# Performance work log

Hardware: AMD Instinct MI355X
Metric: run time of the kernel (lower is better)

## Reference

```python
import jax, jax.numpy as jnp
import numpy as np

DIM = 2048
HEADS = 16
HD = DIM // HEADS  # 128
EPS = 1e-5


def layernorm(t, w, b):
    # FloatLayerNorm: LayerNorm computed in float32 over last dim
    t32 = t.astype(jnp.float32)
    mu = jnp.mean(t32, axis=-1, keepdims=True)
    var = jnp.mean(jnp.square(t32 - mu), axis=-1, keepdims=True)
    y = (t32 - mu) * jax.lax.rsqrt(var + EPS)
    return (y * w + b).astype(t.dtype)


def rope(t, f_real, f_imag):
    # t: [b, s, h, hd]; frequencies in cis form, sliced to seq length
    b, s, h, hd = t.shape
    tr = t.astype(jnp.float32).reshape(b, s, h, hd // 2, 2)
    xr, xi = tr[..., 0], tr[..., 1]
    fr = f_real[:s][None, :, None, :]  # [1, s, 1, hd/2]
    fi = f_imag[:s][None, :, None, :]
    o_r = xr * fr - xi * fi
    o_i = xr * fi + xi * fr
    return jnp.stack([o_r, o_i], axis=-1).reshape(b, s, h, hd).astype(t.dtype)


def proj_norm_rope(t, Wq, Wk, Wv, qn_w, qn_b, kn_w, kn_b, f_real, f_imag):
    b, s, _ = t.shape
    q = layernorm(t @ Wq, qn_w, qn_b).reshape(b, s, HEADS, HD)
    k = layernorm(t @ Wk, kn_w, kn_b).reshape(b, s, HEADS, HD)
    v = (t @ Wv).reshape(b, s, HEADS, HD)
    q = rope(q, f_real, f_imag)
    k = rope(k, f_real, f_imag)
    return q, k, v


def sdpa(q, k, v, scale):
    # q,k,v: [b, s, h, hd] -> out [b, s, h, hd]
    scores = jnp.einsum('bqhd,bkhd->bhqk', q, k) * scale
    probs = jax.nn.softmax(scores, axis=-1)
    return jnp.einsum('bhqk,bkhd->bqhd', probs, v)


def setup_inputs() -> dict:
    key = jax.random.key(0)
    ks = jax.random.split(key, 14)
    d = {
        'c': jax.random.normal(ks[0], (2, 256, DIM), jnp.float32),
        'x': jax.random.normal(ks[1], (2, 1792, DIM), jnp.float32),
        'f_real': jax.random.normal(ks[2], (2048, HD // 2), jnp.float32),
        'f_imag': jax.random.normal(ks[3], (2048, HD // 2), jnp.float32),
    }
    sc = 1.0 / np.sqrt(DIM)
    for i, name in enumerate(['Wq', 'Wk', 'Wv', 'Wo', 'W2q', 'W2k', 'W2v', 'W2o']):
        d[name] = jax.random.normal(ks[4 + i], (DIM, DIM), jnp.float32) * sc
    for name in ['qn_w', 'kn_w', 'q2n_w', 'k2n_w']:
        d[name] = jnp.ones((DIM,), jnp.float32)
    for name in ['qn_b', 'kn_b', 'q2n_b', 'k2n_b']:
        d[name] = jnp.zeros((DIM,), jnp.float32)
    return d


def reference(c, x, f_real, f_imag, Wq, Wk, Wv, Wo, W2q, W2k, W2v, W2o,
              qn_w, qn_b, kn_w, kn_b, q2n_w, q2n_b, k2n_w, k2n_b):
    s1 = c.shape[1]
    c_q, c_k, c_v = proj_norm_rope(c, Wq, Wk, Wv, qn_w, qn_b, kn_w, kn_b, f_real, f_imag)
    x_q, x_k, x_v = proj_norm_rope(x, W2q, W2k, W2v, q2n_w, q2n_b, k2n_w, k2n_b, f_real, f_imag)
    q = jnp.concatenate([c_q, x_q], axis=1)
    k = jnp.concatenate([c_k, x_k], axis=1)
    v = jnp.concatenate([c_v, x_v], axis=1)
    out = sdpa(q, k, v, scale=1.0 / np.sqrt(HD))  # scale_by_num_heads=True
    b, s, _, _ = out.shape
    out = out.reshape(b, s, DIM)
    c_out = out[:, :s1] @ Wo
    x_out = out[:, s1:] @ W2o
    return c_out, x_out
```

## Files before the change

kernel.cpp:

```cpp
#include <hip/hip_runtime.h>

typedef __attribute__((ext_vector_type(8))) short short8;
typedef __attribute__((ext_vector_type(4))) float f32x4;
typedef __attribute__((ext_vector_type(16))) float f32x16;

#define DEV __device__ __forceinline__

DEV unsigned short f2bf(float f) {
  unsigned int u; __builtin_memcpy(&u, &f, 4);
  u = (u + 0x7FFFu + ((u >> 16) & 1u)) >> 16;
  return (unsigned short)u;
}
DEV float bf2f(unsigned short h) {
  unsigned int u = ((unsigned int)h) << 16;
  float f; __builtin_memcpy(&f, &u, 4);
  return f;
}
DEV unsigned int cvtpk(float lo, float hi_) {
  unsigned int r;
  asm("v_cvt_pk_bf16_f32 %0, %1, %2" : "=v"(r) : "v"(lo), "v"(hi_));
  return r;
}

DEV void gload_lds16(const void* g, void* l) {
  __builtin_amdgcn_global_load_lds(
      (const __attribute__((address_space(1))) void*)g,
      (__attribute__((address_space(3))) void*)l, 16, 0, 0);
}

DEV f32x16 mfma32(short8 a, short8 b, f32x16 c) {
  return __builtin_amdgcn_mfma_f32_32x32x16_bf16(a, b, c, 0, 0, 0);
}
DEV f32x4 mfma16(short8 a, short8 b, f32x4 c) {
  return __builtin_amdgcn_mfma_f32_16x16x32_bf16(a, b, c, 0, 0, 0);
}

__global__ __launch_bounds__(256) void conv_tb(const float* __restrict__ c,
                                               const float* __restrict__ x,
                                               unsigned short* __restrict__ tb) {
  int row = blockIdx.x;
  int b = row >> 11, s = row & 2047;
  const float* src = (s < 256) ? (c + (size_t)(b * 256 + s) * 2048)
                               : (x + (size_t)(b * 1792 + (s - 256)) * 2048);
  int t = threadIdx.x;
  float4 v0 = *(const float4*)&src[t * 8];
  float4 v1 = *(const float4*)&src[t * 8 + 4];
  union { unsigned short us[8]; uint4 u; } pk;
  pk.us[0] = f2bf(v0.x); pk.us[1] = f2bf(v0.y); pk.us[2] = f2bf(v0.z); pk.us[3] = f2bf(v0.w);
  pk.us[4] = f2bf(v1.x); pk.us[5] = f2bf(v1.y); pk.us[6] = f2bf(v1.z); pk.us[7] = f2bf(v1.w);
  *(uint4*)&tb[(size_t)row * 2048 + t * 8] = pk.u;
}

__global__ __launch_bounds__(256) void trans_w(
    const float* __restrict__ w0, const float* __restrict__ w1,
    const float* __restrict__ w2, const float* __restrict__ w3,
    const float* __restrict__ w4, const float* __restrict__ w5,
    const float* __restrict__ w6, const float* __restrict__ w7,
    unsigned short* __restrict__ dstbase) {
  const float* W;
  switch (blockIdx.z) {
    case 0: W = w0; break; case 1: W = w1; break; case 2: W = w2; break; case 3: W = w3; break;
    case 4: W = w4; break; case 5: W = w5; break; case 6: W = w6; break; default: W = w7; break;
  }
  unsigned short* Wt = dstbase + (size_t)blockIdx.z * 2048 * 2048;
  __shared__ float tile[64][65];
  int n0 = blockIdx.x * 64, k0 = blockIdx.y * 64;
  int j = threadIdx.x & 63, i0 = threadIdx.x >> 6;
#pragma unroll
  for (int p = 0; p < 16; ++p) {
    int i = i0 + p * 4;
    tile[i][j] = W[(size_t)(k0 + i) * 2048 + n0 + j];
  }
  __syncthreads();
#pragma unroll
  for (int p = 0; p < 16; ++p) {
    int i = i0 + p * 4;
    Wt[(size_t)(n0 + i) * 2048 + k0 + j] = f2bf(tile[j][i]);
  }
}

DEV void stage_A8(char* ldsAbase, const unsigned short* gtile, int mh, int wid, int lane) {
#pragma unroll
  for (int p = 0; p < 2; ++p) {
    int row0 = mh * 64 + p * 128 + wid * 8;
    int row = row0 + (lane >> 3);
    int u = (lane & 7) ^ (row & 7);
    gload_lds16(gtile + (size_t)row * 2048 + u * 8, ldsAbase + row0 * 128);
  }
}
DEV void stage_B8(char* ldsBbase, const unsigned short* gtile, int nh, int wid, int lane) {
#pragma unroll
  for (int p = 0; p < 2; ++p) {
    int idx = p * 8 + wid;
    int row0 = (idx >> 2) * 64 + nh * 32 + (idx & 3) * 8;
    int row = row0 + (lane >> 3);
    int u = (lane & 7) ^ (row & 7);
    gload_lds16(gtile + (size_t)row * 2048 + u * 8, ldsBbase + row0 * 128);
  }
}

__global__ __launch_bounds__(512, 2) void gemm_qkv3_8ph(
    const unsigned short* __restrict__ A,
    const unsigned short* __restrict__ Wt,
    unsigned short* __restrict__ out) {
  extern __shared__ __align__(16) char ldsc[];
  const size_t M2 = 2048ull * 2048ull;
  int bid = blockIdx.x;
  int sw = (bid & 7) * 48 + (bid >> 3);
  const int which = sw >> 7;
  const int rem = sw & 127;
  const int m0 = (rem >> 3) * 256, n0 = (rem & 7) * 256;
  const unsigned short* Bt = Wt + (size_t)(((m0 & 2047) < 256) ? which : which + 4) * M2;
  unsigned short* C = out + (size_t)which * (4096ull * 2048ull);
  const int tid = threadIdx.x, wid = tid >> 6, lane = tid & 63;
  const int g = lane >> 4, l15 = lane & 15;
  const int wm = wid >> 2, wn = wid & 3;
  const unsigned short* gA = A + (size_t)m0 * 2048;
  const unsigned short* gB = Bt + (size_t)n0 * 2048;

  f32x4 acc[8][4] = {};

  stage_A8(ldsc, gA, 0, wid, lane);
  stage_A8(ldsc, gA, 1, wid, lane);
  stage_B8(ldsc + 32768, gB, 0, wid, lane);
  stage_B8(ldsc + 32768, gB, 1, wid, lane);
  stage_A8(ldsc + 65536, gA + 64, 0, wid, lane);
  stage_B8(ldsc + 98304, gB + 64, 0, wid, lane);
  asm volatile("s_waitcnt vmcnt(4)" ::: "memory");
  __builtin_amdgcn_s_barrier();

  const int NT = 32;
#pragma unroll 1
  for (int t = 0; t < NT; ++t) {
    const int bufOff = (t & 1) << 16;
    char* Ab = ldsc + bufOff;
    char* Bb = ldsc + 32768 + bufOff;
    char* An = ldsc + (bufOff ^ 65536);
    char* Bn = ldsc + 32768 + (bufOff ^ 65536);
    short8 af[4][2], bf0[2][2], bf1[2][2];

#pragma unroll
    for (int m4 = 0; m4 < 4; ++m4)
#pragma unroll
      for (int k2 = 0; k2 < 2; ++k2) {
        int row = wm * 128 + m4 * 16 + l15;
        af[m4][k2] = *(const short8*)(Ab + row * 128 + (((k2 * 4 + g) ^ (row & 7)) << 4));
      }
#pragma unroll
    for (int n2 = 0; n2 < 2; ++n2)
#pragma unroll
      for (int k2 = 0; k2 < 2; ++k2) {
        int row = wn * 64 + n2 * 16 + l15;
        bf0[n2][k2] = *(const short8*)(Bb + row * 128 + (((k2 * 4 + g) ^ (row & 7)) << 4));
      }
    if (t + 1 < NT) stage_B8(Bn, gB + (t + 1) * 64, 1, wid, lane);
    __builtin_amdgcn_s_barrier();
    asm volatile("s_waitcnt lgkmcnt(0)" ::: "memory");
    __builtin_amdgcn_sched_barrier(0);
    __builtin_amdgcn_s_setprio(1);
#pragma unroll
    for (int m4 = 0; m4 < 4; ++m4)
#pragma unroll
      for (int n2 = 0; n2 < 2; ++n2)
#pragma unroll
        for (int k2 = 0; k2 < 2; ++k2)
          acc[m4][n2] = mfma16(af[m4][k2], bf0[n2][k2], acc[m4][n2]);
    __builtin_amdgcn_s_setprio(0);
    __builtin_amdgcn_s_barrier();

#pragma unroll
    for (int n2 = 0; n2 < 2; ++n2)
#pragma unroll
      for (int k2 = 0; k2 < 2; ++k2) {
        int row = wn * 64 + 32 + n2 * 16 + l15;
        bf1[n2][k2] = *(const short8*)(Bb + row * 128 + (((k2 * 4 + g) ^ (row & 7)) << 4));
      }
    if (t + 1 < NT) stage_A8(An, gA + (t + 1) * 64, 1, wid, lane);
    __builtin_amdgcn_s_barrier();
    asm volatile("s_waitcnt lgkmcnt(0)" ::: "memory");
    __builtin_amdgcn_sched_barrier(0);
    __builtin_amdgcn_s_setprio(1);
#pragma unroll
    for (int m4 = 0; m4 < 4; ++m4)
#pragma unroll
      for (int n2 = 0; n2 < 2; ++n2)
#pragma unroll
        for (int k2 = 0; k2 < 2; ++k2)
          acc[m4][2 + n2] = mfma16(af[m4][k2], bf1[n2][k2], acc[m4][2 + n2]);
    __builtin_amdgcn_s_setprio(0);
    __builtin_amdgcn_s_barrier();

#pragma unroll
    for (int m4 = 0; m4 < 4; ++m4)
#pragma unroll
      for (int k2 = 0; k2 < 2; ++k2) {
        int row = wm * 128 + 64 + m4 * 16 + l15;
        af[m4][k2] = *(const short8*)(Ab + row * 128 + (((k2 * 4 + g) ^ (row & 7)) << 4));
      }
    if (t + 2 < NT) stage_A8(Ab, gA + (t + 2) * 64, 0, wid, lane);
    __builtin_amdgcn_s_barrier();
    asm volatile("s_waitcnt lgkmcnt(0)" ::: "memory");
    __builtin_amdgcn_sched_barrier(0);
    __builtin_amdgcn_s_setprio(1);
#pragma unroll
    for (int m4 = 0; m4 < 4; ++m4)
#pragma unroll
      for (int n2 = 0; n2 < 2; ++n2)
#pragma unroll
        for (int k2 = 0; k2 < 2; ++k2)
          acc[4 + m4][n2] = mfma16(af[m4][k2], bf0[n2][k2], acc[4 + m4][n2]);
    __builtin_amdgcn_s_setprio(0);
    __builtin_amdgcn_s_barrier();

    if (t + 2 < NT) stage_B8(Bb, gB + (t + 2) * 64, 0, wid, lane);
    __builtin_amdgcn_s_barrier();
    __builtin_amdgcn_s_setprio(1);
#pragma unroll
    for (int m4 = 0; m4 < 4; ++m4)
#pragma unroll
      for (int n2 = 0; n2 < 2; ++n2)
#pragma unroll
        for (int k2 = 0; k2 < 2; ++k2)
          acc[4 + m4][2 + n2] = mfma16(af[m4][k2], bf1[n2][k2], acc[4 + m4][2 + n2]);
    __builtin_amdgcn_s_setprio(0);
    if (t + 2 < NT) {
      asm volatile("s_waitcnt vmcnt(4)" ::: "memory");
    } else if (t + 1 < NT) {
      asm volatile("s_waitcnt vmcnt(0)" ::: "memory");
    }
    __builtin_amdgcn_s_barrier();
  }

#pragma unroll
  for (int mh = 0; mh < 2; ++mh)
#pragma unroll
    for (int m4 = 0; m4 < 4; ++m4)
#pragma unroll
      for (int r = 0; r < 4; ++r) {
        int row = m0 + wm * 128 + mh * 64 + m4 * 16 + 4 * g + r;
#pragma unroll
        for (int nh = 0; nh < 2; ++nh)
#pragma unroll
          for (int n2 = 0; n2 < 2; ++n2)
            C[(size_t)row * 2048 + n0 + wn * 64 + nh * 32 + n2 * 16 + l15] =
                f2bf(acc[mh * 4 + m4][nh * 2 + n2][r]);
      }
}

__global__ __launch_bounds__(256) void gemm_out(
    const unsigned short* __restrict__ A,
    const unsigned short* __restrict__ B1t,
    const unsigned short* __restrict__ B2t,
    float* __restrict__ Co) {
  __shared__ __align__(16) unsigned short As[128 * 32];
  __shared__ __align__(16) unsigned short Bs[128 * 32];
  const int m0 = blockIdx.y * 128, n0 = blockIdx.x * 128;
  const unsigned short* Bt = ((m0 & 2047) < 256) ? B1t : B2t;
  const int tid = threadIdx.x, wid = tid >> 6, lane = tid & 63;
  const int g = lane >> 4, l15 = lane & 15;
  const int wm = wid >> 1, wn = wid & 1;
  const int srow = lane >> 2, skk = (lane & 3) * 8;
  f32x4 acc[4][4] = {};
  for (int k0 = 0; k0 < 2048; k0 += 32) {
#pragma unroll
    for (int rep = 0; rep < 2; ++rep) {
      int ia = wid * 2 + rep;
      gload_lds16(&A[(size_t)(m0 + ia * 16 + srow) * 2048 + k0 + skk], (char*)As + ia * 1024);
      gload_lds16(&Bt[(size_t)(n0 + ia * 16 + srow) * 2048 + k0 + skk], (char*)Bs + ia * 1024);
    }
    __syncthreads();
    short8 a[4], bb[4];
#pragma unroll
    for (int mf = 0; mf < 4; ++mf) a[mf] = *(const short8*)&As[(wm * 64 + mf * 16 + l15) * 32 + g * 8];
#pragma unroll
    for (int nf = 0; nf < 4; ++nf) bb[nf] = *(const short8*)&Bs[(wn * 64 + nf * 16 + l15) * 32 + g * 8];
#pragma unroll
    for (int mf = 0; mf < 4; ++mf)
#pragma unroll
      for (int nf = 0; nf < 4; ++nf)
        acc[mf][nf] = __builtin_amdgcn_mfma_f32_16x16x32_bf16(a[mf], bb[nf], acc[mf][nf], 0, 0, 0);
    __syncthreads();
  }
#pragma unroll
  for (int mf = 0; mf < 4; ++mf)
#pragma unroll
    for (int r = 0; r < 4; ++r) {
      int row = m0 + wm * 64 + mf * 16 + 4 * g + r;
      int b = row >> 11, s = row & 2047;
      size_t dst = (s < 256) ? ((size_t)b * 256 + s) * 2048
                             : 1048576ull + ((size_t)b * 1792 + (s - 256)) * 2048;
#pragma unroll
      for (int nf = 0; nf < 4; ++nf)
        Co[dst + n0 + wn * 64 + nf * 16 + l15] = acc[mf][nf][r];
    }
}

__global__ __launch_bounds__(256) void ln_rope(
    const unsigned short* __restrict__ P,
    const float* __restrict__ w1, const float* __restrict__ b1,
    const float* __restrict__ w2, const float* __restrict__ b2,
    const float* __restrict__ fre, const float* __restrict__ fim,
    unsigned short* __restrict__ Oa, float oscale) {
  int row = blockIdx.x;
  int b = row >> 11, s = row & 2047;
  int pos = (s < 256) ? s : s - 256;
  const float* w = (s < 256) ? w1 : w2;
  const float* bb = (s < 256) ? b1 : b2;
  int t = threadIdx.x, lane = t & 63, wid = t >> 6;
  int col = t * 8;
  uint4 raw = *(const uint4*)&P[(size_t)row * 2048 + col];
  const unsigned short* rp = (const unsigned short*)&raw;
  float xv[8];
#pragma unroll
  for (int j = 0; j < 8; ++j) xv[j] = bf2f(rp[j]);
  float s1 = 0.f, s2 = 0.f;
#pragma unroll
  for (int j = 0; j < 8; ++j) { s1 += xv[j]; s2 += xv[j] * xv[j]; }
#pragma unroll
  for (int off = 32; off; off >>= 1) { s1 += __shfl_xor(s1, off); s2 += __shfl_xor(s2, off); }
  __shared__ float red1[4], red2[4];
  if (lane == 0) { red1[wid] = s1; red2[wid] = s2; }
  __syncthreads();
  s1 = red1[0] + red1[1] + red1[2] + red1[3];
  s2 = red2[0] + red2[1] + red2[2] + red2[3];
  float mean = s1 * (1.f / 2048.f);
  float var = s2 * (1.f / 2048.f) - mean * mean;
  float rs = rsqrtf(var + 1e-5f);
  float4 wv0 = *(const float4*)&w[col], wv1 = *(const float4*)&w[col + 4];
  float4 bv0 = *(const float4*)&bb[col], bv1 = *(const float4*)&bb[col + 4];
  float y[8];
  y[0] = (xv[0] - mean) * rs * wv0.x + bv0.x; y[1] = (xv[1] - mean) * rs * wv0.y + bv0.y;
  y[2] = (xv[2] - mean) * rs * wv0.z + bv0.z; y[3] = (xv[3] - mean) * rs * wv0.w + bv0.w;
  y[4] = (xv[4] - mean) * rs * wv1.x + bv1.x; y[5] = (xv[5] - mean) * rs * wv1.y + bv1.y;
  y[6] = (xv[6] - mean) * rs * wv1.z + bv1.z; y[7] = (xv[7] - mean) * rs * wv1.w + bv1.w;
#pragma unroll
  for (int j = 0; j < 8; ++j) y[j] *= oscale;
  int hd0 = col & 127;
  int i0 = hd0 >> 1;
  float4 fr = *(const float4*)&fre[(size_t)pos * 64 + i0];
  float4 fi = *(const float4*)&fim[(size_t)pos * 64 + i0];
  union { unsigned short us[8]; uint4 u; } pk;
  pk.us[0] = f2bf(y[0] * fr.x - y[1] * fi.x); pk.us[1] = f2bf(y[0] * fi.x + y[1] * fr.x);
  pk.us[2] = f2bf(y[2] * fr.y - y[3] * fi.y); pk.us[3] = f2bf(y[2] * fi.y + y[3] * fr.y);
  pk.us[4] = f2bf(y[4] * fr.z - y[5] * fi.z); pk.us[5] = f2bf(y[4] * fi.z + y[5] * fr.z);
  pk.us[6] = f2bf(y[6] * fr.w - y[7] * fi.w); pk.us[7] = f2bf(y[6] * fi.w + y[7] * fr.w);
  int h = col >> 7;
  *(uint4*)&Oa[((size_t)(b * 16 + h) * 2048 + s) * 128 + hd0] = pk.u;
}

__global__ __launch_bounds__(256) void v_trans(const unsigned short* __restrict__ vp,
                                               unsigned short* __restrict__ va) {
  int bh = blockIdx.y;
  int b = bh >> 4, h = bh & 15;
  int s0 = blockIdx.x * 64;
  __shared__ unsigned short tile[64][128];
  int tid = threadIdx.x;
#pragma unroll
  for (int p = 0; p < 4; ++p) {
    int s = p * 16 + (tid >> 4);
    int d0 = (tid & 15) * 8;
    *(uint4*)&tile[s][d0] = *(const uint4*)&vp[((size_t)b * 2048 + s0 + s) * 2048 + h * 128 + d0];
  }
  __syncthreads();
#pragma unroll
  for (int p = 0; p < 4; ++p) {
    int d = p * 32 + (tid >> 3);
    int soff = (tid & 7) * 8;
    union { unsigned short us[8]; uint4 u; } pk;
#pragma unroll
    for (int u = 0; u < 8; ++u) pk.us[u] = tile[soff + u][d];
    *(uint4*)&va[((size_t)(b * 16 + h) * 128 + d) * 2048 + s0 + soff] = pk.u;
  }
}

#define THR_LOG2 11.5f

__global__ __launch_bounds__(512) void attn_kernel(
    const unsigned short* __restrict__ Q,
    const unsigned short* __restrict__ Kb,
    const unsigned short* __restrict__ Vt,
    unsigned short* __restrict__ O) {
  __shared__ __align__(16) unsigned short smem[32768];
  const int q0 = blockIdx.x * 256;
  const int h = blockIdx.y, b = blockIdx.z;
  const int tid = threadIdx.x, wid = tid >> 6, lane = tid & 63;
  const int l31 = lane & 31, hi = lane >> 5;
  const size_t base = (size_t)(b * 16 + h) * 2048 * 128;
  const unsigned short* kbase = Kb + base;
  const unsigned short* vbase = Vt + base;

  const int qrow = q0 + wid * 32 + l31;
  short8 qf[8];
#pragma unroll
  for (int ks = 0; ks < 8; ++ks)
    qf[ks] = *(const short8*)&Q[base + (size_t)qrow * 128 + ks * 16 + hi * 8];

  f32x16 o_acc[4] = {};
  float m_run = -1e30f, l_run = 0.f;

#define STAGE(cur, kv0)                                                              \
  {                                                                                  \
_Pragma("unroll")                                                                    \
    for (int p = 0; p < 2; ++p) {                                                    \
      int slot = p * 512 + wid * 64 + lane;                                          \
      int row = slot >> 4;                                                           \
      int u = (slot & 15) ^ (row & 7);                                               \
      gload_lds16(&kbase[(size_t)((kv0) + row) * 128 + u * 8],                       \
                  (char*)(smem + (cur) * 16384) + (p * 512 + wid * 64) * 16);        \
    }                                                                                \
_Pragma("unroll")                                                                    \
    for (int p = 0; p < 2; ++p) {                                                    \
      int slot = p * 512 + wid * 64 + lane;                                          \
      int d = slot >> 3;                                                             \
      int u = (slot & 7) ^ (d & 7);                                                  \
      gload_lds16(&vbase[(size_t)d * 2048 + (kv0) + u * 8],                          \
                  (char*)(smem + (cur) * 16384 + 8192) + (p * 512 + wid * 64) * 16); \
    }                                                                                \
  }

  STAGE(0, 0)

#pragma unroll 1
  for (int t = 0; t < 32; ++t) {
    const int cur = t & 1;
    if (t < 31) {
      STAGE(cur ^ 1, (t + 1) * 64)
      asm volatile("s_waitcnt vmcnt(4)" ::: "memory");
    } else {
      asm volatile("s_waitcnt vmcnt(0)" ::: "memory");
    }
    __builtin_amdgcn_s_barrier();

    const char* Ksb = (const char*)(smem + cur * 16384);
    const char* Vsb = (const char*)(smem + cur * 16384 + 8192);

    f32x16 sT0 = {}, sT1 = {};
    __builtin_amdgcn_s_setprio(1);
#pragma unroll
    for (int ks = 0; ks < 8; ++ks) {
      int unit = ks * 2 + hi;
      int r0 = l31;
      short8 kf0 = *(const short8*)(Ksb + ((r0 * 16 + (unit ^ (r0 & 7))) << 4));
      sT0 = mfma32(kf0, qf[ks], sT0);
      int r1 = 32 + l31;
      short8 kf1 = *(const short8*)(Ksb + ((r1 * 16 + (unit ^ (r1 & 7))) << 4));
      sT1 = mfma32(kf1, qf[ks], sT1);
    }
    __builtin_amdgcn_s_setprio(0);

    float mx = sT0[0];
#pragma unroll
    for (int r = 1; r < 16; ++r) mx = fmaxf(mx, sT0[r]);
#pragma unroll
    for (int r = 0; r < 16; ++r) mx = fmaxf(mx, sT1[r]);
    mx = fmaxf(mx, __shfl_xor(mx, 32));
    if (!__all(mx <= m_run + THR_LOG2)) {
      float mn = fmaxf(m_run, mx);
      float corr = __builtin_exp2f(m_run - mn);
      m_run = mn;
      l_run *= corr;
#pragma unroll
      for (int di = 0; di < 4; ++di)
#pragma unroll
        for (int r = 0; r < 16; ++r) o_acc[di][r] *= corr;
    }
    float ts = 0.f;
#pragma unroll
    for (int r = 0; r < 16; ++r) { sT0[r] = __builtin_exp2f(sT0[r] - m_run); ts += sT0[r]; }
#pragma unroll
    for (int r = 0; r < 16; ++r) { sT1[r] = __builtin_exp2f(sT1[r] - m_run); ts += sT1[r]; }
    ts += __shfl_xor(ts, 32);
    l_run += ts;

    unsigned int w0[8], w1[8];
#pragma unroll
    for (int j = 0; j < 8; ++j) {
      w0[j] = cvtpk(sT0[2 * j], sT0[2 * j + 1]);
      w1[j] = cvtpk(sT1[2 * j], sT1[2 * j + 1]);
    }
    unsigned int y0[4], y1[4];
    y0[0] = __shfl_xor((int)(hi ? w0[0] : w0[2]), 32);
    y0[1] = __shfl_xor((int)(hi ? w0[1] : w0[3]), 32);
    y0[2] = __shfl_xor((int)(hi ? w0[4] : w0[6]), 32);
    y0[3] = __shfl_xor((int)(hi ? w0[5] : w0[7]), 32);
    y1[0] = __shfl_xor((int)(hi ? w1[0] : w1[2]), 32);
    y1[1] = __shfl_xor((int)(hi ? w1[1] : w1[3]), 32);
    y1[2] = __shfl_xor((int)(hi ? w1[4] : w1[6]), 32);
    y1[3] = __shfl_xor((int)(hi ? w1[5] : w1[7]), 32);
    union { unsigned int u[4]; short8 s8; } pf[2][2];
    pf[0][0].u[0] = hi ? y0[0] : w0[0]; pf[0][0].u[1] = hi ? y0[1] : w0[1];
    pf[0][0].u[2] = hi ? w0[2] : y0[0]; pf[0][0].u[3] = hi ? w0[3] : y0[1];
    pf[0][1].u[0] = hi ? y0[2] : w0[4]; pf[0][1].u[1] = hi ? y0[3] : w0[5];
    pf[0][1].u[2] = hi ? w0[6] : y0[2]; pf[0][1].u[3] = hi ? w0[7] : y0[3];
    pf[1][0].u[0] = hi ? y1[0] : w1[0]; pf[1][0].u[1] = hi ? y1[1] : w1[1];
    pf[1][0].u[2] = hi ? w1[2] : y1[0]; pf[1][0].u[3] = hi ? w1[3] : y1[1];
    pf[1][1].u[0] = hi ? y1[2] : w1[4]; pf[1][1].u[1] = hi ? y1[3] : w1[5];
    pf[1][1].u[2] = hi ? w1[6] : y1[2]; pf[1][1].u[3] = hi ? w1[7] : y1[3];

    __builtin_amdgcn_s_setprio(1);
#pragma unroll
    for (int di = 0; di < 4; ++di) {
      int row = di * 32 + l31;
      int sw = row & 7;
#pragma unroll
      for (int kb = 0; kb < 2; ++kb)
#pragma unroll
        for (int ks2 = 0; ks2 < 2; ++ks2) {
          int unit = kb * 4 + ks2 * 2 + hi;
          short8 vf = *(const short8*)(Vsb + ((row * 8 + (unit ^ sw)) << 4));
          o_acc[di] = mfma32(vf, pf[kb][ks2].s8, o_acc[di]);
        }
    }
    __builtin_amdgcn_s_setprio(0);
    __builtin_amdgcn_s_barrier();
  }

  float inv = 1.0f / l_run;
  char* ow = (char*)smem + wid * 8192;
#pragma unroll
  for (int di = 0; di < 4; ++di)
#pragma unroll
    for (int rg = 0; rg < 4; ++rg) {
      unsigned int lo = cvtpk(o_acc[di][rg * 4 + 0] * inv, o_acc[di][rg * 4 + 1] * inv);
      unsigned int hi_w = cvtpk(o_acc[di][rg * 4 + 2] * inv, o_acc[di][rg * 4 + 3] * inv);
      int byte = (l31 * 256 + di * 64 + rg * 16 + hi * 8) ^ ((l31 & 7) << 4);
      *(unsigned long long*)(ow + byte) =
          ((unsigned long long)hi_w << 32) | (unsigned long long)lo;
    }
  size_t obase = ((size_t)b * 2048 + q0 + wid * 32) * 2048 + (size_t)h * 128;
#pragma unroll
  for (int it = 0; it < 8; ++it) {
    int q = it * 4 + (lane >> 4);
    int d0 = (lane & 15) * 8;
    int byte = (q * 256 + d0 * 2) ^ ((q & 7) << 4);
    uint4 val = *(const uint4*)(ow + byte);
    *(uint4*)&O[obase + (size_t)q * 2048 + d0] = val;
  }
}

extern "C" void kernel_launch(void* const* d_in, const int* in_sizes, int n_in,
                              void* d_out, int out_size, void* d_ws, size_t ws_size,
                              hipStream_t stream) {
  (void)in_sizes; (void)n_in; (void)out_size; (void)ws_size;
  const float* c = (const float*)d_in[0];
  const float* x = (const float*)d_in[1];
  const float* fre = (const float*)d_in[2];
  const float* fim = (const float*)d_in[3];

  char* ws = (char*)d_ws;
  const size_t M2 = 2048ull * 2048ull;
  unsigned short* tb = (unsigned short*)ws;
  unsigned short* Wt = (unsigned short*)(ws + 16777216ull);
  unsigned short* qkv = (unsigned short*)(ws + 83886080ull);
  unsigned short* qp = qkv;
  unsigned short* kp = (unsigned short*)(ws + 100663296ull);
  unsigned short* vp = (unsigned short*)(ws + 117440512ull);
  unsigned short* qa = (unsigned short*)(ws + 134217728ull);
  unsigned short* ka = (unsigned short*)(ws + 150994944ull);
  unsigned short* va = (unsigned short*)(ws + 167772160ull);
  unsigned short* attn_out = qp;

  (void)hipFuncSetAttribute((const void*)gemm_qkv3_8ph,
                            hipFuncAttributeMaxDynamicSharedMemorySize, 131072);

  conv_tb<<<4096, 256, 0, stream>>>(c, x, tb);
  trans_w<<<dim3(32, 32, 8), 256, 0, stream>>>(
      (const float*)d_in[4], (const float*)d_in[5], (const float*)d_in[6], (const float*)d_in[7],
      (const float*)d_in[8], (const float*)d_in[9], (const float*)d_in[10], (const float*)d_in[11],
      Wt);
  gemm_qkv3_8ph<<<384, 512, 131072, stream>>>(tb, Wt, qkv);
  ln_rope<<<4096, 256, 0, stream>>>(qp, (const float*)d_in[12], (const float*)d_in[16],
                                    (const float*)d_in[14], (const float*)d_in[18], fre, fim, qa,
                                    0.08838834764831845f * 1.4426950408889634f);
  ln_rope<<<4096, 256, 0, stream>>>(kp, (const float*)d_in[13], (const float*)d_in[17],
                                    (const float*)d_in[15], (const float*)d_in[19], fre, fim, ka,
                                    1.0f);
  v_trans<<<dim3(32, 32), 256, 0, stream>>>(vp, va);
  attn_kernel<<<dim3(8, 16, 2), 512, 0, stream>>>(qa, ka, va, attn_out);
  gemm_out<<<dim3(16, 32), 256, 0, stream>>>(attn_out, Wt + 3 * M2, Wt + 7 * M2, (float*)d_out);
}
```

Before: 349.5 us.

## Software-pipeline LDS fragment reads across MFMA quadrants and fewer barriers in QKV GEMM

Restructures the QKV projection GEMM main loop so A and B LDS fragment reads for the next quadrant or tile are issued before the current MFMA quadrant runs. Partial lgkmcnt waits replace full drains, and the per-tile barrier count drops from seven to three. The goal is to hide LDS read latency behind MFMA work and cut synchronisation stalls. In exchange it holds a second A fragment set in registers, raising register pressure, and depends on fragile vmcnt/lgkmcnt counts for correctness against the double-buffered LDS writes.

```diff
diff --git a/kernel.cpp b/kernel.cpp
--- a/kernel.cpp
+++ b/kernel.cpp
@@ -119,6 +119,37 @@
   const unsigned short* gB = Bt + (size_t)n0 * 2048;
 
   f32x4 acc[8][4] = {};
+  short8 afA[4][2], afB[4][2], bf0[2][2], bf1[2][2];
+
+#define READ_AFA(Abase)                                                              \
+  _Pragma("unroll") for (int m4 = 0; m4 < 4; ++m4)                                   \
+  _Pragma("unroll") for (int k2 = 0; k2 < 2; ++k2) {                                 \
+    int row = wm * 128 + m4 * 16 + l15;                                              \
+    afA[m4][k2] = *(const short8*)((Abase) + row * 128 + (((k2 * 4 + g) ^ (row & 7)) << 4)); \
+  }
+#define READ_AFB(Abase)                                                              \
+  _Pragma("unroll") for (int m4 = 0; m4 < 4; ++m4)                                   \
+  _Pragma("unroll") for (int k2 = 0; k2 < 2; ++k2) {                                 \
+    int row = wm * 128 + 64 + m4 * 16 + l15;                                         \
+    afB[m4][k2] = *(const short8*)((Abase) + row * 128 + (((k2 * 4 + g) ^ (row & 7)) << 4)); \
+  }
+#define READ_BF0(Bbase)                                                              \
+  _Pragma("unroll") for (int n2 = 0; n2 < 2; ++n2)                                   \
+  _Pragma("unroll") for (int k2 = 0; k2 < 2; ++k2) {                                 \
+    int row = wn * 64 + n2 * 16 + l15;                                               \
+    bf0[n2][k2] = *(const short8*)((Bbase) + row * 128 + (((k2 * 4 + g) ^ (row & 7)) << 4)); \
+  }
+#define READ_BF1(Bbase)                                                              \
+  _Pragma("unroll") for (int n2 = 0; n2 < 2; ++n2)                                   \
+  _Pragma("unroll") for (int k2 = 0; k2 < 2; ++k2) {                                 \
+    int row = wn * 64 + 32 + n2 * 16 + l15;                                          \
+    bf1[n2][k2] = *(const short8*)((Bbase) + row * 128 + (((k2 * 4 + g) ^ (row & 7)) << 4)); \
+  }
+#define MFMA_Q(mb, AF, BF, cb)                                                       \
+  _Pragma("unroll") for (int m4 = 0; m4 < 4; ++m4)                                   \
+  _Pragma("unroll") for (int n2 = 0; n2 < 2; ++n2)                                   \
+  _Pragma("unroll") for (int k2 = 0; k2 < 2; ++k2)                                   \
+    acc[(mb) + m4][(cb) + n2] = mfma16(AF[m4][k2], BF[n2][k2], acc[(mb) + m4][(cb) + n2]);
 
   stage_A8(ldsc, gA, 0, wid, lane);
   stage_A8(ldsc, gA, 1, wid, lane);
@@ -128,6 +159,8 @@
   stage_B8(ldsc + 98304, gB + 64, 0, wid, lane);
   asm volatile("s_waitcnt vmcnt(4)" ::: "memory");
   __builtin_amdgcn_s_barrier();
+  READ_AFA(ldsc);
+  READ_BF0(ldsc + 32768);
 
   const int NT = 32;
 #pragma unroll 1
@@ -137,95 +170,46 @@
     char* Bb = ldsc + 32768 + bufOff;
     char* An = ldsc + (bufOff ^ 65536);
     char* Bn = ldsc + 32768 + (bufOff ^ 65536);
-    short8 af[4][2], bf0[2][2], bf1[2][2];
-
-#pragma unroll
-    for (int m4 = 0; m4 < 4; ++m4)
-#pragma unroll
-      for (int k2 = 0; k2 < 2; ++k2) {
-        int row = wm * 128 + m4 * 16 + l15;
-        af[m4][k2] = *(const short8*)(Ab + row * 128 + (((k2 * 4 + g) ^ (row & 7)) << 4));
-      }
-#pragma unroll
-    for (int n2 = 0; n2 < 2; ++n2)
-#pragma unroll
-      for (int k2 = 0; k2 < 2; ++k2) {
-        int row = wn * 64 + n2 * 16 + l15;
-        bf0[n2][k2] = *(const short8*)(Bb + row * 128 + (((k2 * 4 + g) ^ (row & 7)) << 4));
-      }
+
+    READ_BF1(Bb);
     if (t + 1 < NT) stage_B8(Bn, gB + (t + 1) * 64, 1, wid, lane);
+    asm volatile("s_waitcnt lgkmcnt(4)" ::: "memory");
+    __builtin_amdgcn_sched_barrier(0);
+    __builtin_amdgcn_s_setprio(1);
+    MFMA_Q(0, afA, bf0, 0)
+    __builtin_amdgcn_s_setprio(0);
+    asm volatile("s_waitcnt vmcnt(6)" ::: "memory");
     __builtin_amdgcn_s_barrier();
+
+    READ_AFB(Ab);
+    if (t + 1 < NT) stage_A8(An, gA + (t + 1) * 64, 1, wid, lane);
+    asm volatile("s_waitcnt lgkmcnt(8)" ::: "memory");
+    __builtin_amdgcn_sched_barrier(0);
+    __builtin_amdgcn_s_setprio(1);
+    MFMA_Q(0, afA, bf1, 2)
+    __builtin_amdgcn_s_setprio(0);
+
+    if (t + 2 < NT) stage_A8(Ab, gA + (t + 2) * 64, 0, wid, lane);
     asm volatile("s_waitcnt lgkmcnt(0)" ::: "memory");
     __builtin_amdgcn_sched_barrier(0);
     __builtin_amdgcn_s_setprio(1);
-#pragma unroll
-    for (int m4 = 0; m4 < 4; ++m4)
-#pragma unroll
-      for (int n2 = 0; n2 < 2; ++n2)
-#pragma unroll
-        for (int k2 = 0; k2 < 2; ++k2)
-          acc[m4][n2] = mfma16(af[m4][k2], bf0[n2][k2], acc[m4][n2]);
+    MFMA_Q(4, afB, bf0, 0)
     __builtin_amdgcn_s_setprio(0);
+    asm volatile("s_waitcnt vmcnt(6)" ::: "memory");
     __builtin_amdgcn_s_barrier();
 
-#pragma unroll
-    for (int n2 = 0; n2 < 2; ++n2)
-#pragma unroll
-      for (int k2 = 0; k2 < 2; ++k2) {
-        int row = wn * 64 + 32 + n2 * 16 + l15;
-        bf1[n2][k2] = *(const short8*)(Bb + row * 128 + (((k2 * 4 + g) ^ (row & 7)) << 4));
-      }
-    if (t + 1 < NT) stage_A8(An, gA + (t + 1) * 64, 1, wid, lane);
-    __builtin_amdgcn_s_barrier();
-    asm volatile("s_waitcnt lgkmcnt(0)" ::: "memory");
+    if (t + 1 < NT) {
+      READ_AFA(An);
+      READ_BF0(Bn);
+    }
+    if (t + 2 < NT) stage_B8(Bb, gB + (t + 2) * 64, 0, wid, lane);
     __builtin_amdgcn_sched_barrier(0);
     __builtin_amdgcn_s_setprio(1);
-#pragma unroll
-    for (int m4 = 0; m4 < 4; ++m4)
-#pragma unroll
-      for (int n2 = 0; n2 < 2; ++n2)
-#pragma unroll
-        for (int k2 = 0; k2 < 2; ++k2)
-          acc[m4][2 + n2] = mfma16(af[m4][k2], bf1[n2][k2], acc[m4][2 + n2]);
-    __builtin_amdgcn_s_setprio(0);
-    __builtin_amdgcn_s_barrier();
-
-#pragma unroll
-    for (int m4 = 0; m4 < 4; ++m4)
-#pragma unroll
-      for (int k2 = 0; k2 < 2; ++k2) {
-        int row = wm * 128 + 64 + m4 * 16 + l15;
-        af[m4][k2] = *(const short8*)(Ab + row * 128 + (((k2 * 4 + g) ^ (row & 7)) << 4));
-      }
-    if (t + 2 < NT) stage_A8(Ab, gA + (t + 2) * 64, 0, wid, lane);
-    __builtin_amdgcn_s_barrier();
-    asm volatile("s_waitcnt lgkmcnt(0)" ::: "memory");
-    __builtin_amdgcn_sched_barrier(0);
-    __builtin_amdgcn_s_setprio(1);
-#pragma unroll
-    for (int m4 = 0; m4 < 4; ++m4)
-#pragma unroll
-      for (int n2 = 0; n2 < 2; ++n2)
-#pragma unroll
-        for (int k2 = 0; k2 < 2; ++k2)
-          acc[4 + m4][n2] = mfma16(af[m4][k2], bf0[n2][k2], acc[4 + m4][n2]);
-    __builtin_amdgcn_s_setprio(0);
-    __builtin_amdgcn_s_barrier();
-
-    if (t + 2 < NT) stage_B8(Bb, gB + (t + 2) * 64, 0, wid, lane);
-    __builtin_amdgcn_s_barrier();
-    __builtin_amdgcn_s_setprio(1);
-#pragma unroll
-    for (int m4 = 0; m4 < 4; ++m4)
-#pragma unroll
-      for (int n2 = 0; n2 < 2; ++n2)
-#pragma unroll
-        for (int k2 = 0; k2 < 2; ++k2)
-          acc[4 + m4][2 + n2] = mfma16(af[m4][k2], bf1[n2][k2], acc[4 + m4][2 + n2]);
+    MFMA_Q(4, afB, bf1, 2)
     __builtin_amdgcn_s_setprio(0);
     if (t + 2 < NT) {
-      asm volatile("s_waitcnt vmcnt(4)" ::: "memory");
-    } else if (t + 1 < NT) {
+      asm volatile("s_waitcnt vmcnt(6)" ::: "memory");
+    } else {
       asm volatile("s_waitcnt vmcnt(0)" ::: "memory");
     }
     __builtin_amdgcn_s_barrier();
@@ -245,6 +229,11 @@
             C[(size_t)row * 2048 + n0 + wn * 64 + nh * 32 + n2 * 16 + l15] =
                 f2bf(acc[mh * 4 + m4][nh * 2 + n2][r]);
       }
+#undef READ_AFA
+#undef READ_AFB
+#undef READ_BF0
+#undef READ_BF1
+#undef MFMA_Q
 }
 
 __global__ __launch_bounds__(256) void gemm_out(
```

Result: faster. 341.7 us (-2.2%).
